# Kernel optimization log

Hardware: AMD Instinct MI355X
Metric: run time of the kernel (lower is better)

The kernel has to match this reference:

```python
import jax, jax.numpy as jnp
import numpy as np

N = 50000
EPS = 1e-4
NUM_CLASSES = 10
PROTOS_PER_CLASS = 5


def setup_inputs() -> dict:
    key = jax.random.key(0)
    ks = jax.random.split(key, 12)
    x = jax.random.normal(ks[0], (N, 512), dtype=jnp.float32)
    edge_index = jax.random.randint(ks[1], (2, 640000), 0, N, dtype=jnp.int64)
    # GCNConv weights (PyG: y = x @ W^T + b after aggregation)
    def glorot(k, o, i):
        s = jnp.sqrt(6.0 / (o + i)).astype(jnp.float32)
        return jax.random.uniform(k, (o, i), jnp.float32, -s, s)
    W1 = glorot(ks[2], 128, 512); b1 = jnp.zeros((128,), jnp.float32)
    W2 = glorot(ks[3], 128, 128); b2 = jnp.zeros((128,), jnp.float32)
    W3 = glorot(ks[4], 128, 128); b3 = jnp.zeros((128,), jnp.float32)
    prototype_vectors = jax.random.uniform(ks[5], (NUM_CLASSES * PROTOS_PER_CLASS, 128), jnp.float32)
    # last layer: +1 for prototype's own class, -0.5 elsewhere, no bias
    proto_class = jnp.arange(NUM_CLASSES * PROTOS_PER_CLASS) // PROTOS_PER_CLASS  # [P]
    identity = (proto_class[None, :] == jnp.arange(NUM_CLASSES)[:, None]).astype(jnp.float32)  # [C,P]
    last_w = 1.0 * identity + (-0.5) * (1.0 - identity)
    return {"x": x, "edge_index": edge_index, "W1": W1, "b1": b1, "W2": W2,
            "b2": b2, "W3": W3, "b3": b3,
            "prototype_vectors": prototype_vectors, "last_w": last_w}


def _gcn_conv(h, src, dst, deg_inv_sqrt, W, b):
    # h: [N,Fin]; messages from src -> dst with symmetric norm; self-loops included in src/dst
    m = h @ W.T                                   # [N,Fout]
    norm = deg_inv_sqrt[src] * deg_inv_sqrt[dst]  # [E+N]
    out = jax.ops.segment_sum(norm[:, None] * m[src], dst, num_segments=N)
    return out + b


def reference(x, edge_index, W1, b1, W2, b2, W3, b3, prototype_vectors, last_w):
    # add self loops once; degree computed on targets (PyG gcn_norm)
    loop = jnp.arange(N, dtype=edge_index.dtype)
    src = jnp.concatenate([edge_index[0], loop])
    dst = jnp.concatenate([edge_index[1], loop])
    deg = jax.ops.segment_sum(jnp.ones_like(src, dtype=x.dtype), dst, num_segments=N)
    deg_inv_sqrt = jnp.where(deg > 0, jax.lax.rsqrt(deg), 0.0)

    h = jax.nn.relu(_gcn_conv(x, src, dst, deg_inv_sqrt, W1, b1))
    h = jax.nn.relu(_gcn_conv(h, src, dst, deg_inv_sqrt, W2, b2))
    h = jax.nn.relu(_gcn_conv(h, src, dst, deg_inv_sqrt, W3, b3))
    emb = h  # [N,128]

    xp = emb @ prototype_vectors.T                                    # [N,P]
    distance = (-2.0 * xp + jnp.sum(emb * emb, axis=1, keepdims=True)
                + jnp.sum(prototype_vectors * prototype_vectors, axis=1)[None, :])
    similarity = jnp.log((distance + 1.0) / (distance + EPS))         # [N,P]
    logits = similarity @ last_w.T                                    # [N,C]
    probs = jax.nn.softmax(logits, axis=-1)
    return logits, probs, emb, distance
```

## Files before the change

kernel.cpp:

```cpp
#include <hip/hip_runtime.h>
#include <cstdint>
#include <cstddef>

#define NFEAT 128
#define NPROTO 50
#define NCLS 10

typedef __attribute__((ext_vector_type(8))) short short8;
typedef __attribute__((ext_vector_type(4))) float floatx4;
typedef _Float16 halfv8 __attribute__((ext_vector_type(8)));


__global__ __launch_bounds__(256) void count_kernel(const int* __restrict__ dst,
                                                    int* __restrict__ cnt, int E) {
  int e = blockIdx.x * 256 + threadIdx.x;
  if (e < E) atomicAdd(&cnt[dst[e]], 1);
}


__global__ __launch_bounds__(256)
void scan1_kernel(const int* __restrict__ cnt, int* __restrict__ row_ptr,
                  int* __restrict__ btot, int Nn) {
  __shared__ int s[256];
  int t = threadIdx.x;
  int i = blockIdx.x * 256 + t;
  int v = (i < Nn) ? cnt[i] : 0;
  s[t] = v;
  __syncthreads();
#pragma unroll
  for (int off = 1; off < 256; off <<= 1) {
    int add = (t >= off) ? s[t - off] : 0;
    __syncthreads();
    s[t] += add;
    __syncthreads();
  }
  if (i < Nn) row_ptr[i] = s[t] - v;
  if (t == 255) btot[blockIdx.x] = s[255];
}

__global__ __launch_bounds__(256)
void scan2_kernel(const int* __restrict__ btot, int* __restrict__ boff,
                  int* __restrict__ row_ptr, int nb, int Nn) {
  __shared__ int s[256];
  int t = threadIdx.x;
  int v = (t < nb) ? btot[t] : 0;
  s[t] = v;
  __syncthreads();
#pragma unroll
  for (int off = 1; off < 256; off <<= 1) {
    int add = (t >= off) ? s[t - off] : 0;
    __syncthreads();
    s[t] += add;
    __syncthreads();
  }
  if (t < nb) boff[t] = s[t] - v;
  if (t == 255) row_ptr[Nn] = s[255];
}

__global__ __launch_bounds__(256)
void scan3_kernel(int* __restrict__ row_ptr, const int* __restrict__ boff,
                  const int* __restrict__ cnt, float* __restrict__ dis, int Nn) {
  int i = blockIdx.x * 256 + threadIdx.x;
  if (i < Nn) {
    row_ptr[i] += boff[blockIdx.x];
    dis[i] = 1.0f / sqrtf((float)(cnt[i] + 1));
  }
}

__global__ __launch_bounds__(256) void fill_kernel(const int* __restrict__ src,
                                                   const int* __restrict__ dst,
                                                   const int* __restrict__ row_ptr,
                                                   int* __restrict__ cursor,
                                                   int* __restrict__ csr_src, int E) {
  int e = blockIdx.x * 256 + threadIdx.x;
  if (e < E) {
    int d = dst[e];
    int pos = atomicAdd(&cursor[d], 1);
    csr_src[row_ptr[d] + pos] = src[e];
  }
}


__device__ __forceinline__ void split1(float v, unsigned short& h, unsigned short& l) {
  unsigned int b = __float_as_uint(v);
  h = (unsigned short)(b >> 16);
  float r = v - __uint_as_float(b & 0xFFFF0000u);
  l = (unsigned short)(__float_as_uint(r) >> 16);
}

__global__ __launch_bounds__(256) void wconv_kernel(const float* __restrict__ W,
                                                    unsigned short* __restrict__ Wh,
                                                    unsigned short* __restrict__ Wl, int n) {
  int i = blockIdx.x * 256 + threadIdx.x;
  if (i < n) {
    unsigned short h, l;
    split1(W[i], h, l);
    Wh[i] = h; Wl[i] = l;
  }
}

__global__ __launch_bounds__(128)
void psplit_kernel(const float* __restrict__ proto, unsigned short* __restrict__ Ph,
                   unsigned short* __restrict__ Pl, float* __restrict__ pn) {
  int t = threadIdx.x;
  for (int idx = t; idx < 64 * 128; idx += 128) {
    int p = idx >> 7;
    float v = (p < NPROTO) ? proto[p * 128 + (idx & 127)] : 0.f;
    unsigned short h, l;
    split1(v, h, l);
    Ph[idx] = h; Pl[idx] = l;
  }
  if (t < 64) {
    float s = 0.f;
    if (t < NPROTO)
      for (int f = 0; f < 128; ++f) { float v = proto[t * 128 + f]; s += v * v; }
    pn[t] = s;
  }
}


__global__ __launch_bounds__(512, 2)
void gemm_p1(const float* __restrict__ A, const float* __restrict__ dis,
             const unsigned short* __restrict__ Wh, const unsigned short* __restrict__ Wl,
             _Float16* __restrict__ C, int M) {
  __shared__ short8 Wlds[4096];
  int t = threadIdx.x;
  int w = t >> 6, lane = t & 63;
  int col = lane & 15, quad = lane >> 4;
  int ntiles = (M + 31) >> 5;
  int tile = blockIdx.x * 8 + w;
  if (tile >= ntiles) tile = ntiles - 1;
  int m0 = tile * 32;

  floatx4 acc[2][8];
#pragma unroll
  for (int a = 0; a < 2; ++a)
#pragma unroll
    for (int b = 0; b < 8; ++b) acc[a][b] = floatx4{0.f, 0.f, 0.f, 0.f};

  int row[2]; float dsc[2];
#pragma unroll
  for (int mt = 0; mt < 2; ++mt) {
    int r = m0 + mt * 16 + col;
    row[mt] = r < M ? r : M - 1;
    dsc[mt] = dis[row[mt]];
  }

  for (int p = 0; p < 4; ++p) {
    const int kb = p * 128;
    __syncthreads();
#pragma unroll
    for (int i = 0; i < 8; ++i) {
      int u = i * 512 + t;
      int pl_ = u >> 11;
      int v = u & 2047;
      int g = v >> 8, q = (v >> 4) & 15, c = v & 15;
      const unsigned short* srcp = (pl_ ? Wl : Wh) + (size_t)(g * 16 + c) * 512 + kb + q * 8;
      __builtin_amdgcn_global_load_lds(
          (const __attribute__((address_space(1))) void*)srcp,
          (__attribute__((address_space(3))) void*)((char*)Wlds + (size_t)(i * 512 + w * 64) * 16),
          16, 0, 0);
    }
    float4 pf[4][2][2];
#pragma unroll
    for (int c0 = 0; c0 < 4; ++c0)
#pragma unroll
      for (int mt = 0; mt < 2; ++mt) {
        const float* pp = A + (size_t)row[mt] * 512 + kb + c0 * 32 + quad * 8;
        pf[c0][mt][0] = *(const float4*)pp;
        pf[c0][mt][1] = *(const float4*)(pp + 4);
      }
    __syncthreads();

#pragma unroll
    for (int ck = 0; ck < 4; ++ck) {
      short8 ah[2], al[2];
#pragma unroll
      for (int mt = 0; mt < 2; ++mt) {
        float4 va = pf[ck][mt][0];
        float4 vb = pf[ck][mt][1];
        float f[8] = {va.x, va.y, va.z, va.w, vb.x, vb.y, vb.z, vb.w};
#pragma unroll
        for (int j = 0; j < 8; ++j) {
          unsigned short h, l;
          split1(f[j] * dsc[mt], h, l);
          ah[mt][j] = (short)h; al[mt][j] = (short)l;
        }
      }
#pragma unroll
      for (int nt = 0; nt < 8; ++nt) {
        int u = nt * 256 + (ck * 4 + quad) * 16 + col;
        short8 bh = Wlds[u];
        short8 bl = Wlds[2048 + u];
#pragma unroll
        for (int mt = 0; mt < 2; ++mt) {
          acc[mt][nt] = __builtin_amdgcn_mfma_f32_16x16x32_bf16(ah[mt], bh, acc[mt][nt], 0, 0, 0);
          acc[mt][nt] = __builtin_amdgcn_mfma_f32_16x16x32_bf16(al[mt], bh, acc[mt][nt], 0, 0, 0);
          acc[mt][nt] = __builtin_amdgcn_mfma_f32_16x16x32_bf16(ah[mt], bl, acc[mt][nt], 0, 0, 0);
        }
      }
    }
  }

#pragma unroll
  for (int mt = 0; mt < 2; ++mt)
#pragma unroll
    for (int r = 0; r < 4; ++r) {
      int m = m0 + mt * 16 + quad * 4 + r;
      if (m < M) {
#pragma unroll
        for (int nt = 0; nt < 8; ++nt)
          C[(size_t)m * NFEAT + nt * 16 + col] = (_Float16)acc[mt][nt][r];
      }
    }
}


__global__ __launch_bounds__(512, 2)
void gemm_p2(const unsigned short* __restrict__ Ah, const unsigned short* __restrict__ Al,
             const unsigned short* __restrict__ Wh, const unsigned short* __restrict__ Wl,
             _Float16* __restrict__ C, int M) {
  __shared__ short8 Wlds[4096];
  int t = threadIdx.x;
  int w = t >> 6, lane = t & 63;
  int col = lane & 15, quad = lane >> 4;
  int ntiles = (M + 31) >> 5;
  int tile = blockIdx.x * 8 + w;
  if (tile >= ntiles) tile = ntiles - 1;
  int m0 = tile * 32;

  floatx4 acc[2][8];
#pragma unroll
  for (int a = 0; a < 2; ++a)
#pragma unroll
    for (int b = 0; b < 8; ++b) acc[a][b] = floatx4{0.f, 0.f, 0.f, 0.f};

  int row[2];
#pragma unroll
  for (int mt = 0; mt < 2; ++mt) {
    int r = m0 + mt * 16 + col;
    row[mt] = r < M ? r : M - 1;
  }

#pragma unroll
  for (int i = 0; i < 4; ++i) {
    int u = i * 512 + t;
    int g = u >> 8, q = (u >> 4) & 15, c = u & 15;
    size_t off = (size_t)(g * 16 + c) * 128 + q * 8;
    char* dst = (char*)Wlds + (size_t)(i * 512 + w * 64) * 16;
    __builtin_amdgcn_global_load_lds(
        (const __attribute__((address_space(1))) void*)(Wh + off),
        (__attribute__((address_space(3))) void*)dst, 16, 0, 0);
    __builtin_amdgcn_global_load_lds(
        (const __attribute__((address_space(1))) void*)(Wl + off),
        (__attribute__((address_space(3))) void*)(dst + 32768), 16, 0, 0);
  }

  short8 pah[4][2], pal[4][2];
#pragma unroll
  for (int ck = 0; ck < 4; ++ck)
#pragma unroll
    for (int mt = 0; mt < 2; ++mt) {
      size_t off = (size_t)row[mt] * 128 + ck * 32 + quad * 8;
      pah[ck][mt] = *(const short8*)(Ah + off);
      pal[ck][mt] = *(const short8*)(Al + off);
    }

  __syncthreads();

#pragma unroll
  for (int ck = 0; ck < 4; ++ck) {
#pragma unroll
    for (int nt = 0; nt < 8; ++nt) {
      int u = (nt * 16 + ck * 4 + quad) * 16 + col;
      short8 bh = Wlds[u];
      short8 bl = Wlds[2048 + u];
#pragma unroll
      for (int mt = 0; mt < 2; ++mt) {
        acc[mt][nt] = __builtin_amdgcn_mfma_f32_16x16x32_bf16(pah[ck][mt], bh, acc[mt][nt], 0, 0, 0);
        acc[mt][nt] = __builtin_amdgcn_mfma_f32_16x16x32_bf16(pal[ck][mt], bh, acc[mt][nt], 0, 0, 0);
        acc[mt][nt] = __builtin_amdgcn_mfma_f32_16x16x32_bf16(pah[ck][mt], bl, acc[mt][nt], 0, 0, 0);
      }
    }
  }

#pragma unroll
  for (int mt = 0; mt < 2; ++mt)
#pragma unroll
    for (int r = 0; r < 4; ++r) {
      int m = m0 + mt * 16 + quad * 4 + r;
      if (m < M) {
#pragma unroll
        for (int nt = 0; nt < 8; ++nt)
          C[(size_t)m * NFEAT + nt * 16 + col] = (_Float16)acc[mt][nt][r];
      }
    }
}


template<int MODE>
__global__ __launch_bounds__(256)
void agg_kernel(const _Float16* __restrict__ m, const int* __restrict__ row_ptr,
                const int* __restrict__ csr_src, const float* __restrict__ dis,
                const float* __restrict__ bias,
                unsigned int* __restrict__ out_h, unsigned int* __restrict__ out_l,
                float* __restrict__ out_f, int Nn) {
  int t = threadIdx.x;
  int w = t >> 6, lane = t & 63;
  int sub = lane >> 4, l = lane & 15;
  int i = blockIdx.x * 16 + w * 4 + sub;
  if (i >= Nn) return;
  const halfv8* m8 = (const halfv8*)m;
  halfv8 sv = m8[(size_t)i * 16 + l];
  float acc[8];
#pragma unroll
  for (int j = 0; j < 8; ++j) acc[j] = (float)sv[j];
  int e0 = row_ptr[i], e1 = row_ptr[i + 1];
  int e = e0;
  for (; e + 4 <= e1; e += 4) {
    int s0 = csr_src[e], s1 = csr_src[e + 1], s2 = csr_src[e + 2], s3 = csr_src[e + 3];
    halfv8 v0 = m8[(size_t)s0 * 16 + l];
    halfv8 v1 = m8[(size_t)s1 * 16 + l];
    halfv8 v2 = m8[(size_t)s2 * 16 + l];
    halfv8 v3 = m8[(size_t)s3 * 16 + l];
#pragma unroll
    for (int j = 0; j < 8; ++j)
      acc[j] += ((float)v0[j] + (float)v1[j]) + ((float)v2[j] + (float)v3[j]);
  }
  for (; e < e1; ++e) {
    int s = csr_src[e];
    halfv8 v = m8[(size_t)s * 16 + l];
#pragma unroll
    for (int j = 0; j < 8; ++j) acc[j] += (float)v[j];
  }
  float di = dis[i];
  float4 ba = ((const float4*)bias)[l * 2];
  float4 bb = ((const float4*)bias)[l * 2 + 1];
  float bv[8] = {ba.x, ba.y, ba.z, ba.w, bb.x, bb.y, bb.z, bb.w};
  float r[8];
#pragma unroll
  for (int j = 0; j < 8; ++j) r[j] = fmaxf(fmaf(di, acc[j], bv[j]), 0.f);
  if (MODE == 0) {
    unsigned int ph[4], pl[4];
#pragma unroll
    for (int j = 0; j < 4; ++j) {
      unsigned short h0, l0, h1, l1;
      split1(di * r[2 * j], h0, l0);
      split1(di * r[2 * j + 1], h1, l1);
      ph[j] = (unsigned int)h0 | ((unsigned int)h1 << 16);
      pl[j] = (unsigned int)l0 | ((unsigned int)l1 << 16);
    }
    ((uint4*)out_h)[(size_t)i * 16 + l] = make_uint4(ph[0], ph[1], ph[2], ph[3]);
    ((uint4*)out_l)[(size_t)i * 16 + l] = make_uint4(pl[0], pl[1], pl[2], pl[3]);
  } else {
    ((float4*)out_f)[(size_t)i * 32 + l * 2] = make_float4(r[0], r[1], r[2], r[3]);
    ((float4*)out_f)[(size_t)i * 32 + l * 2 + 1] = make_float4(r[4], r[5], r[6], r[7]);
  }
}


__global__ __launch_bounds__(256)
void proto_mfma(const float* __restrict__ emb,
                const unsigned short* __restrict__ Ph, const unsigned short* __restrict__ Pl,
                const float* __restrict__ pn, const float* __restrict__ lastw,
                float* __restrict__ out_logits, float* __restrict__ out_probs,
                float* __restrict__ out_dist, int Nn) {
  __shared__ float simS[64][65];
  int t = threadIdx.x;
  int w = t >> 6, lane = t & 63;
  int col = lane & 15, quad = lane >> 4;
  int m0 = blockIdx.x * 64 + w * 16;
  int row = m0 + col;
  int r0 = row < Nn ? row : Nn - 1;

  floatx4 acc[4];
#pragma unroll
  for (int nt = 0; nt < 4; ++nt) acc[nt] = floatx4{0.f, 0.f, 0.f, 0.f};

  float en = 0.f;
  const float* ap = emb + (size_t)r0 * 128 + quad * 8;
#pragma unroll
  for (int kc = 0; kc < 4; ++kc) {
    float4 va = *(const float4*)(ap + kc * 32);
    float4 vb = *(const float4*)(ap + kc * 32 + 4);
    float f[8] = {va.x, va.y, va.z, va.w, vb.x, vb.y, vb.z, vb.w};
    short8 ah, al;
#pragma unroll
    for (int j = 0; j < 8; ++j) {
      unsigned short h, l;
      split1(f[j], h, l);
      ah[j] = (short)h; al[j] = (short)l;
      en = fmaf(f[j], f[j], en);
    }
#pragma unroll
    for (int nt = 0; nt < 4; ++nt) {
      const unsigned short* bp = Ph + (size_t)(nt * 16 + col) * 128 + kc * 32 + quad * 8;
      const unsigned short* bq = Pl + (size_t)(nt * 16 + col) * 128 + kc * 32 + quad * 8;
      short8 bh = *(const short8*)bp;
      short8 bl = *(const short8*)bq;
      acc[nt] = __builtin_amdgcn_mfma_f32_16x16x32_bf16(ah, bh, acc[nt], 0, 0, 0);
      acc[nt] = __builtin_amdgcn_mfma_f32_16x16x32_bf16(al, bh, acc[nt], 0, 0, 0);
      acc[nt] = __builtin_amdgcn_mfma_f32_16x16x32_bf16(ah, bl, acc[nt], 0, 0, 0);
    }
  }
  en += __shfl_xor(en, 16);
  en += __shfl_xor(en, 32);

  float pnv[4];
#pragma unroll
  for (int nt = 0; nt < 4; ++nt) pnv[nt] = pn[nt * 16 + col];

#pragma unroll
  for (int r = 0; r < 4; ++r) {
    int node = m0 + quad * 4 + r;
    float enr = __shfl(en, quad * 4 + r);
    bool valid = node < Nn;
#pragma unroll
    for (int nt = 0; nt < 4; ++nt) {
      int p = nt * 16 + col;
      float d = enr - 2.f * acc[nt][r] + pnv[nt];
      float sim = (p < NPROTO) ? logf((d + 1.0f) / (d + 1e-4f)) : 0.f;
      simS[w * 16 + quad * 4 + r][p] = sim;
      if (valid && p < NPROTO) out_dist[(size_t)node * NPROTO + p] = d;
    }
  }
  __syncthreads();

  if (t < 64) {
    int node = blockIdx.x * 64 + t;
    if (node < Nn) {
      float sims[NPROTO];
#pragma unroll
      for (int p = 0; p < NPROTO; ++p) sims[p] = simS[t][p];
      float lg[NCLS];
      float mx = -1e30f;
#pragma unroll
      for (int c = 0; c < NCLS; ++c) {
        float s = 0.f;
#pragma unroll
        for (int p = 0; p < NPROTO; ++p) s = fmaf(sims[p], lastw[c * NPROTO + p], s);
        lg[c] = s;
        mx = fmaxf(mx, s);
      }
      float ss = 0.f;
#pragma unroll
      for (int c = 0; c < NCLS; ++c) ss += expf(lg[c] - mx);
      float inv = 1.f / ss;
#pragma unroll
      for (int c = 0; c < NCLS; ++c) {
        out_logits[(size_t)node * NCLS + c] = lg[c];
        out_probs[(size_t)node * NCLS + c] = expf(lg[c] - mx) * inv;
      }
    }
  }
}


extern "C" void kernel_launch(void* const* d_in, const int* in_sizes, int n_in,
                              void* d_out, int out_size, void* d_ws, size_t ws_size,
                              hipStream_t stream) {
  const float* x    = (const float*)d_in[0];
  const int*  eidx  = (const int*)d_in[1];
  const float* W1   = (const float*)d_in[2];
  const float* b1   = (const float*)d_in[3];
  const float* W2   = (const float*)d_in[4];
  const float* b2   = (const float*)d_in[5];
  const float* W3   = (const float*)d_in[6];
  const float* b3   = (const float*)d_in[7];
  const float* prot = (const float*)d_in[8];
  const float* lastw= (const float*)d_in[9];

  const int Nn = in_sizes[0] / 512;
  const int E  = in_sizes[1] / 2;
  const int* esrc = eidx;
  const int* edst = eidx + E;

  float* out        = (float*)d_out;
  float* out_logits = out;
  float* out_probs  = out + (size_t)Nn * NCLS;
  float* out_emb    = out + (size_t)Nn * 2 * NCLS;
  float* out_dist   = out_emb + (size_t)Nn * NFEAT;

  _Float16* mbuf = (_Float16*)d_ws;
  unsigned int* hh = (unsigned int*)(mbuf + (size_t)Nn * NFEAT);
  unsigned int* hl = hh + (size_t)Nn * 64;
  unsigned short* W1h = (unsigned short*)(hl + (size_t)Nn * 64);
  unsigned short* W1l = W1h + 128 * 512;
  unsigned short* W2h = W1l + 128 * 512;
  unsigned short* W2l = W2h + 128 * 128;
  unsigned short* W3h = W2l + 128 * 128;
  unsigned short* W3l = W3h + 128 * 128;
  unsigned short* Ph  = W3l + 128 * 128;
  unsigned short* Pl  = Ph + 64 * 128;
  float* pn    = (float*)(Pl + 64 * 128);
  int* cnt     = (int*)(pn + 64);
  float* dis   = (float*)(cnt + Nn);
  int* row_ptr = (int*)(dis + Nn);
  int* cursor  = row_ptr + Nn + 1;
  int* btot    = cursor + Nn;
  int* boff    = btot + 256;
  int* csr_src = boff + 256;

  const int nb = (Nn + 255) / 256;

  hipMemsetAsync(cnt, 0, Nn * sizeof(int), stream);
  hipMemsetAsync(cursor, 0, Nn * sizeof(int), stream);
  count_kernel<<<(E + 255) / 256, 256, 0, stream>>>(edst, cnt, E);
  scan1_kernel<<<nb, 256, 0, stream>>>(cnt, row_ptr, btot, Nn);
  scan2_kernel<<<1, 256, 0, stream>>>(btot, boff, row_ptr, nb, Nn);
  scan3_kernel<<<nb, 256, 0, stream>>>(row_ptr, boff, cnt, dis, Nn);
  fill_kernel<<<(E + 255) / 256, 256, 0, stream>>>(esrc, edst, row_ptr, cursor, csr_src, E);

  wconv_kernel<<<(128 * 512 + 255) / 256, 256, 0, stream>>>(W1, W1h, W1l, 128 * 512);
  wconv_kernel<<<(128 * 128 + 255) / 256, 256, 0, stream>>>(W2, W2h, W2l, 128 * 128);
  wconv_kernel<<<(128 * 128 + 255) / 256, 256, 0, stream>>>(W3, W3h, W3l, 128 * 128);
  psplit_kernel<<<1, 128, 0, stream>>>(prot, Ph, Pl, pn);

  int ntiles = (Nn + 31) / 32;
  int gblocks = (ntiles + 7) / 8;
  int ablocks = (Nn + 15) / 16;
  gemm_p1<<<gblocks, 512, 0, stream>>>(x, dis, W1h, W1l, mbuf, Nn);
  agg_kernel<0><<<ablocks, 256, 0, stream>>>(mbuf, row_ptr, csr_src, dis, b1, hh, hl, nullptr, Nn);
  gemm_p2<<<gblocks, 512, 0, stream>>>((const unsigned short*)hh, (const unsigned short*)hl,
                                       W2h, W2l, mbuf, Nn);
  agg_kernel<0><<<ablocks, 256, 0, stream>>>(mbuf, row_ptr, csr_src, dis, b2, hh, hl, nullptr, Nn);
  gemm_p2<<<gblocks, 512, 0, stream>>>((const unsigned short*)hh, (const unsigned short*)hl,
                                       W3h, W3l, mbuf, Nn);
  agg_kernel<1><<<ablocks, 256, 0, stream>>>(mbuf, row_ptr, csr_src, dis, b3, nullptr, nullptr, out_emb, Nn);

  proto_mfma<<<(Nn + 63) / 64, 256, 0, stream>>>(out_emb, Ph, Pl, pn, lastw,
                                                 out_logits, out_probs, out_dist, Nn);
}
```

Baseline: 438.3 us.

## Rewrite first GEMM as persistent fp16 kernel with resident weights

The first-layer GEMM now rounds W1 to plain fp16 and splits the activations into fp16 hi/lo pairs. This needs two MFMAs per step instead of three bf16 ones. All of W1 (128 KB) is loaded into LDS once per block, and a persistent grid of 256 blocks × 16 waves strides over 16-row tiles, which removes the per-K-chunk weight reloads and barriers. Each wave software-prefetches its A row chunks 4 steps ahead. The trade-offs are lower precision on W1 (the low part is dropped), 128 KB of LDS per block limiting occupancy to one block per CU, and smaller tiles per wave.

```diff
diff --git a/kernel.cpp b/kernel.cpp
--- a/kernel.cpp
+++ b/kernel.cpp
@@ -99,6 +99,12 @@
   }
 }
 
+__global__ __launch_bounds__(256) void wconv16_kernel(const float* __restrict__ W,
+                                                      _Float16* __restrict__ Wo, int n) {
+  int i = blockIdx.x * 256 + threadIdx.x;
+  if (i < n) Wo[i] = (_Float16)W[i];
+}
+
 __global__ __launch_bounds__(128)
 void psplit_kernel(const float* __restrict__ proto, unsigned short* __restrict__ Ph,
                    unsigned short* __restrict__ Pl, float* __restrict__ pn) {
@@ -119,100 +125,82 @@
 }
 
 
-__global__ __launch_bounds__(512, 2)
+__global__ __launch_bounds__(1024)
 void gemm_p1(const float* __restrict__ A, const float* __restrict__ dis,
-             const unsigned short* __restrict__ Wh, const unsigned short* __restrict__ Wl,
+             const _Float16* __restrict__ W16,
              _Float16* __restrict__ C, int M) {
-  __shared__ short8 Wlds[4096];
+  __shared__ halfv8 Wlds[8192];
   int t = threadIdx.x;
   int w = t >> 6, lane = t & 63;
   int col = lane & 15, quad = lane >> 4;
-  int ntiles = (M + 31) >> 5;
-  int tile = blockIdx.x * 8 + w;
-  if (tile >= ntiles) tile = ntiles - 1;
-  int m0 = tile * 32;
-
-  floatx4 acc[2][8];
-#pragma unroll
-  for (int a = 0; a < 2; ++a)
-#pragma unroll
-    for (int b = 0; b < 8; ++b) acc[a][b] = floatx4{0.f, 0.f, 0.f, 0.f};
-
-  int row[2]; float dsc[2];
-#pragma unroll
-  for (int mt = 0; mt < 2; ++mt) {
-    int r = m0 + mt * 16 + col;
-    row[mt] = r < M ? r : M - 1;
-    dsc[mt] = dis[row[mt]];
-  }
-
-  for (int p = 0; p < 4; ++p) {
-    const int kb = p * 128;
-    __syncthreads();
-#pragma unroll
-    for (int i = 0; i < 8; ++i) {
-      int u = i * 512 + t;
-      int pl_ = u >> 11;
-      int v = u & 2047;
-      int g = v >> 8, q = (v >> 4) & 15, c = v & 15;
-      const unsigned short* srcp = (pl_ ? Wl : Wh) + (size_t)(g * 16 + c) * 512 + kb + q * 8;
-      __builtin_amdgcn_global_load_lds(
-          (const __attribute__((address_space(1))) void*)srcp,
-          (__attribute__((address_space(3))) void*)((char*)Wlds + (size_t)(i * 512 + w * 64) * 16),
-          16, 0, 0);
-    }
-    float4 pf[4][2][2];
-#pragma unroll
-    for (int c0 = 0; c0 < 4; ++c0)
-#pragma unroll
-      for (int mt = 0; mt < 2; ++mt) {
-        const float* pp = A + (size_t)row[mt] * 512 + kb + c0 * 32 + quad * 8;
-        pf[c0][mt][0] = *(const float4*)pp;
-        pf[c0][mt][1] = *(const float4*)(pp + 4);
-      }
-    __syncthreads();
-
-#pragma unroll
-    for (int ck = 0; ck < 4; ++ck) {
-      short8 ah[2], al[2];
-#pragma unroll
-      for (int mt = 0; mt < 2; ++mt) {
-        float4 va = pf[ck][mt][0];
-        float4 vb = pf[ck][mt][1];
-        float f[8] = {va.x, va.y, va.z, va.w, vb.x, vb.y, vb.z, vb.w};
-#pragma unroll
-        for (int j = 0; j < 8; ++j) {
-          unsigned short h, l;
-          split1(f[j] * dsc[mt], h, l);
-          ah[mt][j] = (short)h; al[mt][j] = (short)l;
-        }
+
+#pragma unroll
+  for (int i = 0; i < 8; ++i) {
+    int u = i * 1024 + t;
+    int nt = u >> 10, rest = u & 1023;
+    int ckq = rest >> 4, c = rest & 15;
+    const _Float16* srcp = W16 + (size_t)(nt * 16 + c) * 512 + ckq * 8;
+    __builtin_amdgcn_global_load_lds(
+        (const __attribute__((address_space(1))) void*)srcp,
+        (__attribute__((address_space(3))) void*)((char*)Wlds + (size_t)(i * 1024 + w * 64) * 16),
+        16, 0, 0);
+  }
+  __syncthreads();
+
+  int ntiles = (M + 15) >> 4;
+  for (int tile = blockIdx.x * 16 + w; tile < ntiles; tile += gridDim.x * 16) {
+    int m0 = tile * 16;
+    int r = m0 + col;
+    int row = r < M ? r : M - 1;
+    float dsc = dis[row];
+    const float* ap = A + (size_t)row * 512 + quad * 8;
+
+    floatx4 acc[8];
+#pragma unroll
+    for (int nt = 0; nt < 8; ++nt) acc[nt] = floatx4{0.f, 0.f, 0.f, 0.f};
+
+    float4 pf[4][2];
+#pragma unroll
+    for (int c0 = 0; c0 < 4; ++c0) {
+      pf[c0][0] = *(const float4*)(ap + c0 * 32);
+      pf[c0][1] = *(const float4*)(ap + c0 * 32 + 4);
+    }
+
+#pragma unroll
+    for (int ck = 0; ck < 16; ++ck) {
+      float4 va = pf[ck & 3][0];
+      float4 vb = pf[ck & 3][1];
+      if (ck + 4 < 16) {
+        pf[ck & 3][0] = *(const float4*)(ap + (ck + 4) * 32);
+        pf[ck & 3][1] = *(const float4*)(ap + (ck + 4) * 32 + 4);
+      }
+      float f[8] = {va.x, va.y, va.z, va.w, vb.x, vb.y, vb.z, vb.w};
+      halfv8 ah, al;
+#pragma unroll
+      for (int j = 0; j < 8; ++j) {
+        float s = f[j] * dsc;
+        _Float16 h = (_Float16)s;
+        ah[j] = h;
+        al[j] = (_Float16)(s - (float)h);
       }
 #pragma unroll
       for (int nt = 0; nt < 8; ++nt) {
-        int u = nt * 256 + (ck * 4 + quad) * 16 + col;
-        short8 bh = Wlds[u];
-        short8 bl = Wlds[2048 + u];
-#pragma unroll
-        for (int mt = 0; mt < 2; ++mt) {
-          acc[mt][nt] = __builtin_amdgcn_mfma_f32_16x16x32_bf16(ah[mt], bh, acc[mt][nt], 0, 0, 0);
-          acc[mt][nt] = __builtin_amdgcn_mfma_f32_16x16x32_bf16(al[mt], bh, acc[mt][nt], 0, 0, 0);
-          acc[mt][nt] = __builtin_amdgcn_mfma_f32_16x16x32_bf16(ah[mt], bl, acc[mt][nt], 0, 0, 0);
-        }
-      }
-    }
-  }
-
-#pragma unroll
-  for (int mt = 0; mt < 2; ++mt)
-#pragma unroll
-    for (int r = 0; r < 4; ++r) {
-      int m = m0 + mt * 16 + quad * 4 + r;
+        halfv8 bh = Wlds[nt * 1024 + (ck * 4 + quad) * 16 + col];
+        acc[nt] = __builtin_amdgcn_mfma_f32_16x16x32_f16(ah, bh, acc[nt], 0, 0, 0);
+        acc[nt] = __builtin_amdgcn_mfma_f32_16x16x32_f16(al, bh, acc[nt], 0, 0, 0);
+      }
+    }
+
+#pragma unroll
+    for (int rr = 0; rr < 4; ++rr) {
+      int m = m0 + quad * 4 + rr;
       if (m < M) {
 #pragma unroll
         for (int nt = 0; nt < 8; ++nt)
-          C[(size_t)m * NFEAT + nt * 16 + col] = (_Float16)acc[mt][nt][r];
-      }
-    }
+          C[(size_t)m * NFEAT + nt * 16 + col] = (_Float16)acc[nt][rr];
+      }
+    }
+  }
 }
 
 
@@ -484,9 +472,8 @@
   _Float16* mbuf = (_Float16*)d_ws;
   unsigned int* hh = (unsigned int*)(mbuf + (size_t)Nn * NFEAT);
   unsigned int* hl = hh + (size_t)Nn * 64;
-  unsigned short* W1h = (unsigned short*)(hl + (size_t)Nn * 64);
-  unsigned short* W1l = W1h + 128 * 512;
-  unsigned short* W2h = W1l + 128 * 512;
+  _Float16* W1f = (_Float16*)(hl + (size_t)Nn * 64);
+  unsigned short* W2h = (unsigned short*)(W1f + 128 * 512);
   unsigned short* W2l = W2h + 128 * 128;
   unsigned short* W3h = W2l + 128 * 128;
   unsigned short* W3l = W3h + 128 * 128;
@@ -511,15 +498,15 @@
   scan3_kernel<<<nb, 256, 0, stream>>>(row_ptr, boff, cnt, dis, Nn);
   fill_kernel<<<(E + 255) / 256, 256, 0, stream>>>(esrc, edst, row_ptr, cursor, csr_src, E);
 
-  wconv_kernel<<<(128 * 512 + 255) / 256, 256, 0, stream>>>(W1, W1h, W1l, 128 * 512);
+  wconv16_kernel<<<(128 * 512 + 255) / 256, 256, 0, stream>>>(W1, W1f, 128 * 512);
   wconv_kernel<<<(128 * 128 + 255) / 256, 256, 0, stream>>>(W2, W2h, W2l, 128 * 128);
   wconv_kernel<<<(128 * 128 + 255) / 256, 256, 0, stream>>>(W3, W3h, W3l, 128 * 128);
   psplit_kernel<<<1, 128, 0, stream>>>(prot, Ph, Pl, pn);
 
-  int ntiles = (Nn + 31) / 32;
-  int gblocks = (ntiles + 7) / 8;
+  int ntiles32 = (Nn + 31) / 32;
+  int gblocks = (ntiles32 + 7) / 8;
   int ablocks = (Nn + 15) / 16;
-  gemm_p1<<<gblocks, 512, 0, stream>>>(x, dis, W1h, W1l, mbuf, Nn);
+  gemm_p1<<<256, 1024, 0, stream>>>(x, dis, W1f, mbuf, Nn);
   agg_kernel<0><<<ablocks, 256, 0, stream>>>(mbuf, row_ptr, csr_src, dis, b1, hh, hl, nullptr, Nn);
   gemm_p2<<<gblocks, 512, 0, stream>>>((const unsigned short*)hh, (const unsigned short*)hl,
                                        W2h, W2l, mbuf, Nn);
```

Measured after the change: 606.9 us. 1.38x slower.
